# Kernel tuning notes

Hardware: AMD Instinct MI355X
Metric: run time of the kernel (lower is better)

The kernel has to match this reference:

```python
import jax, jax.numpy as jnp
import numpy as np


def fwht(x):
    """Fast Walsh-Hadamard transform along last axis (n must be a power of 2).
    Loop runs log2(n) times (fixed, ~12 iters) -- fully vectorized butterflies."""
    n = x.shape[-1]
    prefix = x.shape[:-1]
    x = x.reshape(-1, n)
    h = 1
    while h < n:
        x = x.reshape(-1, n // (2 * h), 2, h)
        a, b = x[:, :, 0, :], x[:, :, 1, :]
        x = jnp.stack([a + b, a - b], axis=2).reshape(-1, n)
        h *= 2
    return x.reshape(prefix + (n,))


def setup_inputs() -> dict:
    key = jax.random.key(0)
    ks = jax.random.split(key, 8)
    Bz, S, N, M = 4, 2048, 4096, 4096   # batch, seq, in_features, out_features
    CODESZ, CB_SIZE, RANK = 8, 256, 64
    inp = {}
    inp["input"] = jax.random.normal(ks[0], (Bz, S, N), dtype=jnp.float32)
    inp["Qidxs"] = jax.random.randint(ks[1], (M, N // CODESZ), 0, CB_SIZE, dtype=jnp.int32)
    inp["codebook_vals"] = jax.random.normal(ks[2], (CB_SIZE, CODESZ), dtype=jnp.float32)
    # SU/SV are random sign vectors in QuIP#
    inp["SU"] = jnp.sign(jax.random.normal(ks[3], (N,), dtype=jnp.float32))
    inp["SV"] = jnp.sign(jax.random.normal(ks[4], (M,), dtype=jnp.float32))
    inp["Wscale"] = jnp.ones((), dtype=jnp.float32)
    inp["A"] = jax.random.normal(ks[5], (M, RANK), dtype=jnp.float32) * 0.01
    inp["B"] = jax.random.normal(ks[6], (RANK, N), dtype=jnp.float32) * 0.01
    return inp


def reference(input, Qidxs, codebook_vals, SU, SV, Wscale, A, B):
    n = SU.shape[0]   # in_features
    m = SV.shape[0]   # out_features
    lead = input.shape[:-1]
    x = input.reshape(-1, n).astype(jnp.float32)          # [T, n]
    # input rotation: x <- H^T (x * SU) / sqrt(n)   (matmul_hadUt, K=1 case)
    x = fwht(x * SU) * (1.0 / jnp.sqrt(jnp.float32(n)))
    # low-rank correction branch (rank > 0)
    Bx = x @ B.T                                          # [T, rank]
    # dequantize: codebook lookup [m, n/codesz, codesz] -> [m, n]
    W = codebook_vals[Qidxs].reshape(m, n)
    z = (x @ W.T) * Wscale                                # [T, m]
    z = z + Bx @ A.T
    # output rotation: z <- SV * (H z) / sqrt(m)
    z = fwht(z) * (1.0 / jnp.sqrt(jnp.float32(m))) * SV
    return z.reshape(lead + (m,))
```

## Files before the change

kernel.cpp:

```cpp
#include <hip/hip_runtime.h>
#include <hip/hip_bf16.h>


typedef __attribute__((ext_vector_type(8))) short short8;
typedef __attribute__((ext_vector_type(4))) float f32x4;

#define T_ROWS 8192
#define NDIM   4096
#define MDIM   4096
#define NT     (NDIM / 64)

__device__ __forceinline__ void gld_lds16(const void* g, void* lds_uniform) {
    __builtin_amdgcn_global_load_lds(
        (const __attribute__((address_space(1))) unsigned int*)(unsigned long long)(uintptr_t)g,
        (__attribute__((address_space(3))) unsigned int*)(unsigned int)(uintptr_t)lds_uniform,
        16, 0, 0);
}

__device__ __forceinline__ void bfly(float& a, float& b) {
    float s = a + b, d = a - b; a = s; b = d;
}
__device__ __forceinline__ void bfly4(float4& a, float4& b) {
    bfly(a.x, b.x); bfly(a.y, b.y); bfly(a.z, b.z); bfly(a.w, b.w);
}

__global__ __launch_bounds__(256) void fwht_in_kernel(
        const float* __restrict__ in, const float* __restrict__ SU,
        __hip_bfloat16* __restrict__ xout) {
    __shared__ float sh[4096];
    const int t = threadIdx.x;
    const size_t r = blockIdx.x;
    const float4* src = (const float4*)(in + (r << 12));
    const float4* su4 = (const float4*)SU;

    float4 v[4];
#pragma unroll
    for (int s = 0; s < 4; ++s) {
        float4 a = src[t + (s << 8)];
        float4 u = su4[t + (s << 8)];
        a.x *= u.x; a.y *= u.y; a.z *= u.z; a.w *= u.w;
        v[s] = a;
    }
#pragma unroll
    for (int s = 0; s < 4; ++s) {
        bfly(v[s].x, v[s].y); bfly(v[s].z, v[s].w);
        bfly(v[s].x, v[s].z); bfly(v[s].y, v[s].w);
    }
    bfly4(v[0], v[1]); bfly4(v[2], v[3]);
    bfly4(v[0], v[2]); bfly4(v[1], v[3]);

#pragma unroll
    for (int s = 0; s < 4; ++s) ((float4*)sh)[t + (s << 8)] = v[s];

#pragma unroll
    for (int h = 4; h <= 512; h <<= 1) {
        __syncthreads();
#pragma unroll
        for (int s = 0; s < 8; ++s) {
            int p = t + (s << 8);
            int i = ((p & ~(h - 1)) << 1) | (p & (h - 1));
            float a = sh[i], b = sh[i + h];
            sh[i] = a + b; sh[i + h] = a - b;
        }
    }
    __syncthreads();

    __hip_bfloat16* dst = xout + (r << 12);
    const float sc = 0.015625f;
#pragma unroll
    for (int s = 0; s < 4; ++s) {
        float4 a = ((const float4*)sh)[t + (s << 8)];
        union { __hip_bfloat16 h[4]; unsigned long long u; } pk;
        pk.h[0] = __float2bfloat16(a.x * sc);
        pk.h[1] = __float2bfloat16(a.y * sc);
        pk.h[2] = __float2bfloat16(a.z * sc);
        pk.h[3] = __float2bfloat16(a.w * sc);
        ((unsigned long long*)dst)[t + (s << 8)] = pk.u;
    }
}

__global__ __launch_bounds__(256) void dequant_kernel(
        const int* __restrict__ Qidxs, const float* __restrict__ cb,
        const float* __restrict__ Wscale, const float* __restrict__ A,
        const float* __restrict__ B, __hip_bfloat16* __restrict__ Weff) {
    __shared__ float At[64][68];
    __shared__ float Bs[64][68];
    __shared__ float cbs[2048];
    const int t = threadIdx.x;
    const int i0 = blockIdx.y * 64, j0 = blockIdx.x * 64;

    {
        const float* ga = A + (size_t)i0 * 64;
        const int r = t >> 2, kb = (t & 3) * 16;
#pragma unroll
        for (int j = 0; j < 16; ++j) At[kb + j][r] = ga[t * 16 + j];
        const int k = t >> 2, c0 = (t & 3) * 16;
        const float* gb = B + (size_t)k * NDIM + j0 + c0;
#pragma unroll
        for (int j = 0; j < 16; ++j) Bs[k][c0 + j] = gb[j];
#pragma unroll
        for (int j = 0; j < 8; ++j) cbs[t * 8 + j] = cb[t * 8 + j];
    }
    __syncthreads();

    const int ty = t >> 4, tx = t & 15;
    float acc[4][4];
#pragma unroll
    for (int a = 0; a < 4; ++a)
#pragma unroll
        for (int b = 0; b < 4; ++b) acc[a][b] = 0.f;

#pragma unroll 8
    for (int k = 0; k < 64; ++k) {
        const float4 av = *(const float4*)&At[k][ty * 4];
        const float4 bv = *(const float4*)&Bs[k][tx * 4];
        const float aa[4] = {av.x, av.y, av.z, av.w};
        const float bb[4] = {bv.x, bv.y, bv.z, bv.w};
#pragma unroll
        for (int ii = 0; ii < 4; ++ii)
#pragma unroll
            for (int jj = 0; jj < 4; ++jj) acc[ii][jj] += aa[ii] * bb[jj];
    }

    const float wsc = Wscale[0];
#pragma unroll
    for (int ii = 0; ii < 4; ++ii) {
        const int i = i0 + ty * 4 + ii;
        const int* qrow = Qidxs + (size_t)i * (NDIM / 8);
        union { __hip_bfloat16 h[4]; unsigned long long u; } pk;
#pragma unroll
        for (int jj = 0; jj < 4; ++jj) {
            const int j = j0 + tx * 4 + jj;
            const int idx = qrow[j >> 3];
            const float val = cbs[idx * 8 + (j & 7)] * wsc + acc[ii][jj];
            pk.h[jj] = __float2bfloat16(val);
        }
        *(unsigned long long*)&Weff[(size_t)i * NDIM + j0 + tx * 4] = pk.u;
    }
}

__global__ __launch_bounds__(512, 2) void gemm256_kernel(
        const __hip_bfloat16* __restrict__ X, const __hip_bfloat16* __restrict__ W,
        float* __restrict__ Z) {
    __shared__ short smem[65536];

    const int b = blockIdx.x;
    const int swz = (b & 7) * 64 + (b >> 3);
    const int bm = swz >> 4, bn = swz & 15;

    const int tid = threadIdx.x;
    const int lane = tid & 63, wid = tid >> 6;
    const int wm = wid >> 2, wn = wid & 3;
    const int lr = lane & 15, lk = lane >> 4;
    const int swb = (lr & 7) << 4;
    const int c0 = (((lk << 4)) ^ swb) >> 1;
    const int c1 = ((64 | (lk << 4)) ^ swb) >> 1;
    const int wbase = wid << 9;

    const int grow = tid >> 3;
    const int scol = (((tid & 7) ^ (grow & 7)) << 3);
    const __hip_bfloat16* gA = X + (size_t)(bm * 256 + grow) * NDIM + scol;
    const __hip_bfloat16* gB = W + (size_t)(bn * 256 + grow) * NDIM + scol;

#define STA2(OFS, H, Q, BUF) gld_lds16(gA + (size_t)(((H) * 128 + (Q) * 64) * NDIM) + (OFS), \
        &smem[(BUF) * 32768 + (H) * 8192 + (Q) * 4096 + wbase])
#define STB2(OFS, H, Q, BUF) gld_lds16(gB + (size_t)(((H) * 128 + (Q) * 64) * NDIM) + (OFS), \
        &smem[(BUF) * 32768 + 16384 + (H) * 8192 + (Q) * 4096 + wbase])
#define STAGE_A(OFS, BUF) do { STA2(OFS,0,0,BUF); STA2(OFS,0,1,BUF); \
                               STA2(OFS,1,0,BUF); STA2(OFS,1,1,BUF); } while (0)
#define STAGE_B(OFS, BUF) do { STB2(OFS,0,0,BUF); STB2(OFS,0,1,BUF); \
                               STB2(OFS,1,0,BUF); STB2(OFS,1,1,BUF); } while (0)

#define RDA(D0, D1, D2, D3, M0, AB) do { \
    D0 = *(const short8*)((AB) + ((M0) * 16 + lr) * 64 + c0); \
    D1 = *(const short8*)((AB) + ((M0) * 16 + lr) * 64 + c1); \
    D2 = *(const short8*)((AB) + ((M0) * 16 + 16 + lr) * 64 + c0); \
    D3 = *(const short8*)((AB) + ((M0) * 16 + 16 + lr) * 64 + c1); \
} while (0)

#define RDB(BARR, BUF) do { \
    const short* bB_ = smem + (BUF) * 32768 + 16384 + (wn * 64 + lr) * 64; \
    _Pragma("unroll") \
    for (int n = 0; n < 4; ++n) { \
        BARR[2 * n]     = *(const short8*)(bB_ + n * 1024 + c0); \
        BARR[2 * n + 1] = *(const short8*)(bB_ + n * 1024 + c1); \
    } \
} while (0)

#define MFMA2(A0, A1, E0, E1, M0, BF) do { \
    __builtin_amdgcn_s_setprio(1); \
    _Pragma("unroll") \
    for (int n = 0; n < 4; ++n) \
        acc[M0][n] = __builtin_amdgcn_mfma_f32_16x16x32_bf16(A0, BF[2 * n], acc[M0][n], 0, 0, 0); \
    _Pragma("unroll") \
    for (int n = 0; n < 4; ++n) \
        acc[(M0) + 1][n] = __builtin_amdgcn_mfma_f32_16x16x32_bf16(E0, BF[2 * n], acc[(M0) + 1][n], 0, 0, 0); \
    _Pragma("unroll") \
    for (int n = 0; n < 4; ++n) \
        acc[M0][n] = __builtin_amdgcn_mfma_f32_16x16x32_bf16(A1, BF[2 * n + 1], acc[M0][n], 0, 0, 0); \
    _Pragma("unroll") \
    for (int n = 0; n < 4; ++n) \
        acc[(M0) + 1][n] = __builtin_amdgcn_mfma_f32_16x16x32_bf16(E1, BF[2 * n + 1], acc[(M0) + 1][n], 0, 0, 0); \
    __builtin_amdgcn_s_setprio(0); \
} while (0)

#define TILE(CUR, BF, BN, DO_STA, DO_STB, DO_BN, VMMID, VMEND, DO_ENDBAR) do { \
    const short* aBase = smem + (CUR) * 32768 + wm * 8192; \
    if (DO_STA) STAGE_A(64, 1 - (CUR)); \
    if (DO_STB) STAGE_B(128, (CUR)); \
    RDA(xa0, xa1, xb0, xb1, 0, aBase); \
    RDA(ya0, ya1, yb0, yb1, 2, aBase); \
    MFMA2(xa0, xa1, xb0, xb1, 0, BF); \
    RDA(xa0, xa1, xb0, xb1, 4, aBase); \
    MFMA2(ya0, ya1, yb0, yb1, 2, BF); \
    RDA(ya0, ya1, yb0, yb1, 6, aBase); \
    if (DO_BN) { \
        asm volatile("s_waitcnt vmcnt(" #VMMID ")" ::: "memory"); \
        RDB(BN, 1 - (CUR)); \
    } \
    MFMA2(xa0, xa1, xb0, xb1, 4, BF); \
    MFMA2(ya0, ya1, yb0, yb1, 6, BF); \
    asm volatile("s_waitcnt lgkmcnt(0)" ::: "memory"); \
    asm volatile("s_waitcnt vmcnt(" #VMEND ")" ::: "memory"); \
    if (DO_ENDBAR) __builtin_amdgcn_s_barrier(); \
    gA += 64; gB += 64; \
} while (0)

    f32x4 acc[8][4];
#pragma unroll
    for (int m = 0; m < 8; ++m)
#pragma unroll
        for (int n = 0; n < 4; ++n) acc[m][n] = 0.f;

    short8 B0r[8], B1r[8];
    short8 xa0, xa1, xb0, xb1, ya0, ya1, yb0, yb1;

    STAGE_A(0, 0);
    STAGE_B(0, 0);
    STAGE_B(64, 1);
    asm volatile("s_waitcnt vmcnt(4)" ::: "memory");
    __builtin_amdgcn_s_barrier();
    RDB(B0r, 0);
    asm volatile("s_waitcnt lgkmcnt(0)" ::: "memory");
    __builtin_amdgcn_s_barrier();

    for (int i = 0; i < 31; ++i) {
        TILE(0, B0r, B1r, 1, 1, 1, 8, 4, 1);
        TILE(1, B1r, B0r, 1, 1, 1, 8, 4, 1);
    }
    TILE(0, B0r, B1r, 1, 0, 1, 4, 0, 1);
    TILE(1, B1r, B0r, 0, 0, 0, 0, 0, 0);

    const size_t r0 = (size_t)bm * 256 + wm * 128 + (lk << 2);
    const size_t cb0 = (size_t)bn * 256 + wn * 64 + lr;
#pragma unroll
    for (int m = 0; m < 8; ++m)
#pragma unroll
        for (int n = 0; n < 4; ++n) {
            const size_t col = cb0 + n * 16;
#pragma unroll
            for (int j = 0; j < 4; ++j)
                Z[(r0 + m * 16 + j) * MDIM + col] = acc[m][n][j];
        }
}

__global__ __launch_bounds__(256) void fwht_out_kernel(
        float* __restrict__ z, const float* __restrict__ SV) {
    __shared__ float sh[4096];
    const int t = threadIdx.x;
    const size_t r = blockIdx.x;
    float4* row = (float4*)(z + (r << 12));
    const float4* sv4 = (const float4*)SV;

    float4 v[4];
#pragma unroll
    for (int s = 0; s < 4; ++s) v[s] = row[t + (s << 8)];
#pragma unroll
    for (int s = 0; s < 4; ++s) {
        bfly(v[s].x, v[s].y); bfly(v[s].z, v[s].w);
        bfly(v[s].x, v[s].z); bfly(v[s].y, v[s].w);
    }
    bfly4(v[0], v[1]); bfly4(v[2], v[3]);
    bfly4(v[0], v[2]); bfly4(v[1], v[3]);

#pragma unroll
    for (int s = 0; s < 4; ++s) ((float4*)sh)[t + (s << 8)] = v[s];

#pragma unroll
    for (int h = 4; h <= 512; h <<= 1) {
        __syncthreads();
#pragma unroll
        for (int s = 0; s < 8; ++s) {
            int p = t + (s << 8);
            int i = ((p & ~(h - 1)) << 1) | (p & (h - 1));
            float a = sh[i], b = sh[i + h];
            sh[i] = a + b; sh[i + h] = a - b;
        }
    }
    __syncthreads();

    const float sc = 0.015625f;
#pragma unroll
    for (int s = 0; s < 4; ++s) {
        float4 a = ((const float4*)sh)[t + (s << 8)];
        float4 u = sv4[t + (s << 8)];
        a.x = a.x * sc * u.x; a.y = a.y * sc * u.y;
        a.z = a.z * sc * u.z; a.w = a.w * sc * u.w;
        row[t + (s << 8)] = a;
    }
}

extern "C" void kernel_launch(void* const* d_in, const int* in_sizes, int n_in,
                              void* d_out, int out_size, void* d_ws, size_t ws_size,
                              hipStream_t stream) {
    const float* input  = (const float*)d_in[0];
    const int*   Qidxs  = (const int*)d_in[1];
    const float* cbvals = (const float*)d_in[2];
    const float* SU     = (const float*)d_in[3];
    const float* SV     = (const float*)d_in[4];
    const float* Wscale = (const float*)d_in[5];
    const float* A      = (const float*)d_in[6];
    const float* B      = (const float*)d_in[7];
    float* out = (float*)d_out;

    __hip_bfloat16* xbf = (__hip_bfloat16*)d_ws;
    __hip_bfloat16* wbf = (__hip_bfloat16*)((char*)d_ws + (size_t)T_ROWS * NDIM * 2);

    fwht_in_kernel<<<T_ROWS, 256, 0, stream>>>(input, SU, xbf);
    dequant_kernel<<<dim3(MDIM / 64, MDIM / 64), 256, 0, stream>>>(
        Qidxs, cbvals, Wscale, A, B, wbf);
    gemm256_kernel<<<(T_ROWS / 256) * (MDIM / 256), 512, 0, stream>>>(xbf, wbf, out);
    fwht_out_kernel<<<T_ROWS, 256, 0, stream>>>(out, SV);
}
```

Before: 385.5 us.

## Use radix-16 register FWHT and prefetch next-tile A fragments in GEMM

The 4096-point Walsh-Hadamard kernels now run three radix-16 register passes with two padded-LDS transposes, replacing nine shared-memory butterfly stages that each needed a barrier. The GEMM main loop is re-pipelined: fragment 0 of the next A tile is read from LDS before the current tile ends, and the barrier moves to just before the next-buffer reads. This cuts LDS traffic and barriers in the FWHT and aims to hide LDS latency in the GEMM. The trade-offs are strided bf16 scalar global stores in fwht_in and more delicate waitcnt and barrier placement.

```diff
diff --git a/kernel.cpp b/kernel.cpp
--- a/kernel.cpp
+++ b/kernel.cpp
@@ -20,63 +20,87 @@
 __device__ __forceinline__ void bfly(float& a, float& b) {
     float s = a + b, d = a - b; a = s; b = d;
 }
-__device__ __forceinline__ void bfly4(float4& a, float4& b) {
-    bfly(a.x, b.x); bfly(a.y, b.y); bfly(a.z, b.z); bfly(a.w, b.w);
+
+__device__ __forceinline__ void fwht16(float* v) {
+#pragma unroll
+    for (int h = 1; h <= 8; h <<= 1)
+#pragma unroll
+        for (int j = 0; j < 16; ++j)
+            if (!(j & h)) bfly(v[j], v[j | h]);
 }
 
 __global__ __launch_bounds__(256) void fwht_in_kernel(
         const float* __restrict__ in, const float* __restrict__ SU,
         __hip_bfloat16* __restrict__ xout) {
-    __shared__ float sh[4096];
+    __shared__ float sh[4352];
     const int t = threadIdx.x;
     const size_t r = blockIdx.x;
-    const float4* src = (const float4*)(in + (r << 12));
-    const float4* su4 = (const float4*)SU;
-
-    float4 v[4];
-#pragma unroll
-    for (int s = 0; s < 4; ++s) {
-        float4 a = src[t + (s << 8)];
-        float4 u = su4[t + (s << 8)];
-        a.x *= u.x; a.y *= u.y; a.z *= u.z; a.w *= u.w;
-        v[s] = a;
-    }
-#pragma unroll
-    for (int s = 0; s < 4; ++s) {
-        bfly(v[s].x, v[s].y); bfly(v[s].z, v[s].w);
-        bfly(v[s].x, v[s].z); bfly(v[s].y, v[s].w);
-    }
-    bfly4(v[0], v[1]); bfly4(v[2], v[3]);
-    bfly4(v[0], v[2]); bfly4(v[1], v[3]);
-
-#pragma unroll
-    for (int s = 0; s < 4; ++s) ((float4*)sh)[t + (s << 8)] = v[s];
-
-#pragma unroll
-    for (int h = 4; h <= 512; h <<= 1) {
-        __syncthreads();
-#pragma unroll
-        for (int s = 0; s < 8; ++s) {
-            int p = t + (s << 8);
-            int i = ((p & ~(h - 1)) << 1) | (p & (h - 1));
-            float a = sh[i], b = sh[i + h];
-            sh[i] = a + b; sh[i + h] = a - b;
+    float v[16];
+    {
+        const float4* s4 = (const float4*)(in + (r << 12) + t * 16);
+        const float4* u4 = (const float4*)(SU + t * 16);
+#pragma unroll
+        for (int q = 0; q < 4; ++q) {
+            float4 a = s4[q], u = u4[q];
+            v[4 * q + 0] = a.x * u.x; v[4 * q + 1] = a.y * u.y;
+            v[4 * q + 2] = a.z * u.z; v[4 * q + 3] = a.w * u.w;
         }
     }
-    __syncthreads();
-
+    fwht16(v);
+#pragma unroll
+    for (int j = 0; j < 16; ++j) sh[17 * t + j] = v[j];
+    __syncthreads();
+    const int baseB = (t & 15) + 272 * (t >> 4);
+#pragma unroll
+    for (int j = 0; j < 16; ++j) v[j] = sh[baseB + 17 * j];
+    fwht16(v);
+#pragma unroll
+    for (int j = 0; j < 16; ++j) sh[baseB + 17 * j] = v[j];
+    __syncthreads();
+    const int baseC = t + (t >> 4);
+#pragma unroll
+    for (int j = 0; j < 16; ++j) v[j] = sh[baseC + 272 * j];
+    fwht16(v);
     __hip_bfloat16* dst = xout + (r << 12);
-    const float sc = 0.015625f;
-#pragma unroll
-    for (int s = 0; s < 4; ++s) {
-        float4 a = ((const float4*)sh)[t + (s << 8)];
-        union { __hip_bfloat16 h[4]; unsigned long long u; } pk;
-        pk.h[0] = __float2bfloat16(a.x * sc);
-        pk.h[1] = __float2bfloat16(a.y * sc);
-        pk.h[2] = __float2bfloat16(a.z * sc);
-        pk.h[3] = __float2bfloat16(a.w * sc);
-        ((unsigned long long*)dst)[t + (s << 8)] = pk.u;
-    }
+#pragma unroll
+    for (int j = 0; j < 16; ++j)
+        dst[(j << 8) + t] = __float2bfloat16(v[j] * 0.015625f);
+}
+
+__global__ __launch_bounds__(256) void fwht_out_kernel(
+        float* __restrict__ z, const float* __restrict__ SV) {
+    __shared__ float sh[4352];
+    const int t = threadIdx.x;
+    const size_t r = blockIdx.x;
+    float* row = z + (r << 12);
+    float v[16];
+    {
+        const float4* s4 = (const float4*)(row + t * 16);
+#pragma unroll
+        for (int q = 0; q < 4; ++q) {
+            float4 a = s4[q];
+            v[4 * q + 0] = a.x; v[4 * q + 1] = a.y;
+            v[4 * q + 2] = a.z; v[4 * q + 3] = a.w;
+        }
+    }
+    fwht16(v);
+#pragma unroll
+    for (int j = 0; j < 16; ++j) sh[17 * t + j] = v[j];
+    __syncthreads();
+    const int baseB = (t & 15) + 272 * (t >> 4);
+#pragma unroll
+    for (int j = 0; j < 16; ++j) v[j] = sh[baseB + 17 * j];
+    fwht16(v);
+#pragma unroll
+    for (int j = 0; j < 16; ++j) sh[baseB + 17 * j] = v[j];
+    __syncthreads();
+    const int baseC = t + (t >> 4);
+#pragma unroll
+    for (int j = 0; j < 16; ++j) v[j] = sh[baseC + 272 * j];
+    fwht16(v);
+#pragma unroll
+    for (int j = 0; j < 16; ++j)
+        row[(j << 8) + t] = v[j] * 0.015625f * SV[(j << 8) + t];
 }
 
 __global__ __launch_bounds__(256) void dequant_kernel(
@@ -204,25 +228,28 @@
     __builtin_amdgcn_s_setprio(0); \
 } while (0)
 
-#define TILE(CUR, BF, BN, DO_STA, DO_STB, DO_BN, VMMID, VMEND, DO_ENDBAR) do { \
+#define TILE(CUR, BF, BN, DO_STA, DO_STB, DO_PF, VMMID, LAST) do { \
     const short* aBase = smem + (CUR) * 32768 + wm * 8192; \
     if (DO_STA) STAGE_A(64, 1 - (CUR)); \
     if (DO_STB) STAGE_B(128, (CUR)); \
-    RDA(xa0, xa1, xb0, xb1, 0, aBase); \
-    RDA(ya0, ya1, yb0, yb1, 2, aBase); \
-    MFMA2(xa0, xa1, xb0, xb1, 0, BF); \
-    RDA(xa0, xa1, xb0, xb1, 4, aBase); \
-    MFMA2(ya0, ya1, yb0, yb1, 2, BF); \
-    RDA(ya0, ya1, yb0, yb1, 6, aBase); \
-    if (DO_BN) { \
+    RDA(t0, t1, t2, t3, 2, aBase); \
+    MFMA2(p0, p1, p2, p3, 0, BF); \
+    RDA(p0, p1, p2, p3, 4, aBase); \
+    MFMA2(t0, t1, t2, t3, 2, BF); \
+    RDA(t0, t1, t2, t3, 6, aBase); \
+    MFMA2(p0, p1, p2, p3, 4, BF); \
+    if (DO_PF) { \
         asm volatile("s_waitcnt vmcnt(" #VMMID ")" ::: "memory"); \
+        __builtin_amdgcn_s_barrier(); \
         RDB(BN, 1 - (CUR)); \
+        RDA(p0, p1, p2, p3, 0, smem + (1 - (CUR)) * 32768 + wm * 8192); \
+        __builtin_amdgcn_sched_barrier(0); \
     } \
-    MFMA2(xa0, xa1, xb0, xb1, 4, BF); \
-    MFMA2(ya0, ya1, yb0, yb1, 6, BF); \
-    asm volatile("s_waitcnt lgkmcnt(0)" ::: "memory"); \
-    asm volatile("s_waitcnt vmcnt(" #VMEND ")" ::: "memory"); \
-    if (DO_ENDBAR) __builtin_amdgcn_s_barrier(); \
+    MFMA2(t0, t1, t2, t3, 6, BF); \
+    if (!(LAST)) { \
+        asm volatile("s_waitcnt lgkmcnt(0)" ::: "memory"); \
+        __builtin_amdgcn_s_barrier(); \
+    } \
     gA += 64; gB += 64; \
 } while (0)
 
@@ -233,7 +260,7 @@
         for (int n = 0; n < 4; ++n) acc[m][n] = 0.f;
 
     short8 B0r[8], B1r[8];
-    short8 xa0, xa1, xb0, xb1, ya0, ya1, yb0, yb1;
+    short8 p0, p1, p2, p3, t0, t1, t2, t3;
 
     STAGE_A(0, 0);
     STAGE_B(0, 0);
@@ -241,15 +268,16 @@
     asm volatile("s_waitcnt vmcnt(4)" ::: "memory");
     __builtin_amdgcn_s_barrier();
     RDB(B0r, 0);
+    RDA(p0, p1, p2, p3, 0, smem + wm * 8192);
     asm volatile("s_waitcnt lgkmcnt(0)" ::: "memory");
     __builtin_amdgcn_s_barrier();
 
     for (int i = 0; i < 31; ++i) {
-        TILE(0, B0r, B1r, 1, 1, 1, 8, 4, 1);
-        TILE(1, B1r, B0r, 1, 1, 1, 8, 4, 1);
-    }
-    TILE(0, B0r, B1r, 1, 0, 1, 4, 0, 1);
-    TILE(1, B1r, B0r, 0, 0, 0, 0, 0, 0);
+        TILE(0, B0r, B1r, 1, 1, 1, 4, 0);
+        TILE(1, B1r, B0r, 1, 1, 1, 4, 0);
+    }
+    TILE(0, B0r, B1r, 1, 0, 1, 0, 0);
+    TILE(1, B1r, B0r, 0, 0, 0, 0, 1);
 
     const size_t r0 = (size_t)bm * 256 + wm * 128 + (lk << 2);
     const size_t cb0 = (size_t)bn * 256 + wn * 64 + lr;
@@ -262,52 +290,6 @@
             for (int j = 0; j < 4; ++j)
                 Z[(r0 + m * 16 + j) * MDIM + col] = acc[m][n][j];
         }
-}
-
-__global__ __launch_bounds__(256) void fwht_out_kernel(
-        float* __restrict__ z, const float* __restrict__ SV) {
-    __shared__ float sh[4096];
-    const int t = threadIdx.x;
-    const size_t r = blockIdx.x;
-    float4* row = (float4*)(z + (r << 12));
-    const float4* sv4 = (const float4*)SV;
-
-    float4 v[4];
-#pragma unroll
-    for (int s = 0; s < 4; ++s) v[s] = row[t + (s << 8)];
-#pragma unroll
-    for (int s = 0; s < 4; ++s) {
-        bfly(v[s].x, v[s].y); bfly(v[s].z, v[s].w);
-        bfly(v[s].x, v[s].z); bfly(v[s].y, v[s].w);
-    }
-    bfly4(v[0], v[1]); bfly4(v[2], v[3]);
-    bfly4(v[0], v[2]); bfly4(v[1], v[3]);
-
-#pragma unroll
-    for (int s = 0; s < 4; ++s) ((float4*)sh)[t + (s << 8)] = v[s];
-
-#pragma unroll
-    for (int h = 4; h <= 512; h <<= 1) {
-        __syncthreads();
-#pragma unroll
-        for (int s = 0; s < 8; ++s) {
-            int p = t + (s << 8);
-            int i = ((p & ~(h - 1)) << 1) | (p & (h - 1));
-            float a = sh[i], b = sh[i + h];
-            sh[i] = a + b; sh[i + h] = a - b;
-        }
-    }
-    __syncthreads();
-
-    const float sc = 0.015625f;
-#pragma unroll
-    for (int s = 0; s < 4; ++s) {
-        float4 a = ((const float4*)sh)[t + (s << 8)];
-        float4 u = sv4[t + (s << 8)];
-        a.x = a.x * sc * u.x; a.y = a.y * sc * u.y;
-        a.z = a.z * sc * u.z; a.w = a.w * sc * u.w;
-        row[t + (s << 8)] = a;
-    }
 }
 
 extern "C" void kernel_launch(void* const* d_in, const int* in_sizes, int n_in,
```

Result: no change. 379.5 us (-1.6%).
